# Performance work log

Measured on AMD Instinct MI355X. Metric: run time of the kernel, lower is better.

The kernel has to match this reference:

```python
import jax, jax.numpy as jnp
import numpy as np

B, S, HID = 1, 2048, 1024
H, HKV, D = 16, 4, 64
THETA = 10000.0


def _rope_tables(seq_len, head_dim):
    # Matches RotaryEmbedding: emb = cat(freqs, freqs); kernel reads cos/sin at even
    # positions d for each rotated pair (d, d+1), i.e. columns 0::2 of the table.
    inv_freq = 1.0 / (THETA ** (jnp.arange(0, head_dim, 2, dtype=jnp.float32) / head_dim))
    freqs = jnp.arange(seq_len, dtype=jnp.float32)[:, None] * inv_freq[None, :]  # [S, D/2]
    emb = jnp.concatenate([freqs, freqs], axis=-1)  # [S, D]
    return jnp.cos(emb)[:, 0::2], jnp.sin(emb)[:, 0::2]  # each [S, D/2]


def _apply_rope(x, cos, sin):
    # x: [B, H, S, D]; rotate interleaved pairs (2i, 2i+1) as in the kernel.
    xe, xo = x[..., 0::2], x[..., 1::2]
    re = xe * cos - xo * sin
    ro = xe * sin + xo * cos
    return jnp.stack([re, ro], axis=-1).reshape(x.shape)


def setup_inputs() -> dict:
    key = jax.random.key(0)
    k0, k1, k2, k3, k4 = jax.random.split(key, 5)
    return {
        "hidden_states": jax.random.normal(k0, (B, S, HID), dtype=jnp.float32),
        "Wq": jax.random.normal(k1, (HID, H * D), dtype=jnp.float32) * 0.02,
        "Wk": jax.random.normal(k2, (HID, HKV * D), dtype=jnp.float32) * 0.02,
        "Wv": jax.random.normal(k3, (HID, HKV * D), dtype=jnp.float32) * 0.02,
        "Wo": jax.random.normal(k4, (H * D, HID), dtype=jnp.float32) * 0.02,
    }


def reference(hidden_states, Wq, Wk, Wv, Wo):
    b, s, _ = hidden_states.shape
    q = (hidden_states @ Wq).reshape(b, s, H, D).transpose(0, 2, 1, 3)    # [B,H,S,D]
    k = (hidden_states @ Wk).reshape(b, s, HKV, D).transpose(0, 2, 1, 3)  # [B,Hkv,S,D]
    v = (hidden_states @ Wv).reshape(b, s, HKV, D).transpose(0, 2, 1, 3)

    cos, sin = _rope_tables(s, D)
    q = _apply_rope(q, cos, sin)
    k = _apply_rope(k, cos, sin)

    G = H // HKV  # GQA group size: query head h -> kv head h // G
    qg = q.reshape(b, HKV, G, s, D)
    scale = jnp.float32(D) ** -0.5
    scores = jnp.einsum("bkgqd,bkpd->bkgqp", qg, k) * scale  # [B,Hkv,G,S,S]
    causal = jnp.tril(jnp.ones((s, s), dtype=bool))
    scores = jnp.where(causal, scores, jnp.float32(-1e30))
    probs = jax.nn.softmax(scores, axis=-1)
    out = jnp.einsum("bkgqp,bkpd->bkgqd", probs, v).reshape(b, H, s, D)
    out = out.transpose(0, 2, 1, 3).reshape(b, s, H * D)
    return out @ Wo
```

## Files before the change

kernel.cpp:

```cpp
#include <hip/hip_runtime.h>
#include <hip/hip_bf16.h>
#include <math.h>

#define SEQ   2048
#define HID   1024
#define NH    16
#define NKV   4
#define DH    64
#define GQ    (NH / NKV)
#define NQKV  1536
#define KT    64
#define QB    32
#define CH    512
#define NCH   (SEQ / CH)
#define PSTR  72
#define LNSC  0.2878231366f
#define GS    528
#define BUFS  (8 * GS)
#define QSCALE 0.18033688011112042f

typedef __attribute__((ext_vector_type(8))) short bf16x8;
typedef __attribute__((ext_vector_type(4))) float f32x4;
typedef unsigned short u16;
typedef unsigned int u32;

__device__ __forceinline__ u16 f2bf(float f) {
    union { float f; unsigned u; } x; x.f = f;
    unsigned r = x.u + 0x7fffu + ((x.u >> 16) & 1u);
    return (u16)(r >> 16);
}
__device__ __forceinline__ u32 cvtpk(float lo, float hi) {
    u32 r;
    asm("v_cvt_pk_bf16_f32 %0, %1, %2" : "=v"(r) : "v"(lo), "v"(hi));
    return r;
}
__device__ __forceinline__ void load_lds16(const u16* g, u16* l) {
    __builtin_amdgcn_global_load_lds(
        (const __attribute__((address_space(1))) unsigned int*)g,
        (__attribute__((address_space(3))) unsigned int*)l, 16, 0, 0);
}

__global__ __launch_bounds__(256) void setup(const float* __restrict__ X,
                                             const float* __restrict__ Wq,
                                             const float* __restrict__ Wk,
                                             const float* __restrict__ Wv,
                                             const float* __restrict__ Wo,
                                             u16* __restrict__ Xb,
                                             u16* __restrict__ Wt,
                                             u16* __restrict__ WoT) {
    const int z = blockIdx.z;
    if (z == 4) {
        const int idx = ((int)blockIdx.y * 64 + (int)blockIdx.x) * 256 + threadIdx.x;
        const float4 v = ((const float4*)X)[idx];
        ushort4 o;
        o.x = f2bf(v.x); o.y = f2bf(v.y); o.z = f2bf(v.z); o.w = f2bf(v.w);
        ((ushort4*)Xb)[idx] = o;
        return;
    }
    const float* in; u16* out; int N;
    if (z == 0)      { in = Wq; out = Wt;                             N = HID; }
    else if (z == 1) { in = Wk; out = Wt + (size_t)HID * HID;         N = 256; }
    else if (z == 2) { in = Wv; out = Wt + (size_t)(HID + 256) * HID; N = 256; }
    else             { in = Wo; out = WoT;                            N = HID; }

    const int n0 = blockIdx.x * 32;
    if (n0 >= N) return;
    const int k0 = blockIdx.y * 32;

    __shared__ float t[32][33];
    const int tx = threadIdx.x & 31;
    const int ty = threadIdx.x >> 5;
    #pragma unroll
    for (int i = 0; i < 4; ++i)
        t[ty + i * 8][tx] = in[(size_t)(k0 + ty + i * 8) * N + n0 + tx];
    __syncthreads();
    #pragma unroll
    for (int i = 0; i < 4; ++i)
        out[(size_t)(n0 + ty + i * 8) * HID + k0 + tx] = f2bf(t[tx][ty + i * 8]);
}

__global__ __launch_bounds__(256, 3) void gemm_qkv(const u16* __restrict__ A,
                                                   const u16* __restrict__ Bt,
                                                   u16* __restrict__ Qb,
                                                   u16* __restrict__ Kb,
                                                   u16* __restrict__ VTg) {
    __shared__ u16 Bs[4 * BUFS];

    const int tid  = threadIdx.x;
    const int lane = tid & 63;
    const int w    = tid >> 6;
    const int c    = lane & 15;
    const int quad = lane >> 4;
    const int m0   = blockIdx.y * 64;
    const int n0   = blockIdx.x * 64;

    const int rr8 = lane >> 3;
    const int cc8 = lane & 7;
    const u16* gB0 = Bt + (size_t)(n0 + w * 16 + rr8) * HID + ((cc8 ^ rr8) * 8);
    const u16* gB1 = gB0 + (size_t)8 * HID;
    const int  gofs0 = (w * 2) * GS, gofs1 = (w * 2 + 1) * GS;

    const u16* gA = A + (size_t)(m0 + w * 16 + c) * HID + quad * 8;
    const int bbase = (c >> 3) * GS + (c & 7) * 64;
    int bsw[2];
    #pragma unroll
    for (int ks = 0; ks < 2; ++ks)
        bsw[ks] = bbase + (((ks * 4 + quad) ^ (c & 7)) * 8);

    f32x4 acc[4];
    #pragma unroll
    for (int nt = 0; nt < 4; ++nt) acc[nt] = (f32x4){0.f, 0.f, 0.f, 0.f};

    bf16x8 afc[2], afB[2], afn[2];
    afc[0] = *(const bf16x8*)gA;
    afc[1] = *(const bf16x8*)(gA + 32);
    load_lds16(gB0,      &Bs[0 * BUFS + gofs0]);
    load_lds16(gB1,      &Bs[0 * BUFS + gofs1]);
    load_lds16(gB0 + 64, &Bs[1 * BUFS + gofs0]);
    load_lds16(gB1 + 64, &Bs[1 * BUFS + gofs1]);

    const int NI = HID / 128;
    for (int i = 0; i < NI; ++i) {
        const int t0 = 2 * i;
        __syncthreads();
        if (i + 1 < NI) {
            load_lds16(gB0 + (t0 + 2) * 64, &Bs[((t0 + 2) & 3) * BUFS + gofs0]);
            load_lds16(gB1 + (t0 + 2) * 64, &Bs[((t0 + 2) & 3) * BUFS + gofs1]);
            load_lds16(gB0 + (t0 + 3) * 64, &Bs[((t0 + 3) & 3) * BUFS + gofs0]);
            load_lds16(gB1 + (t0 + 3) * 64, &Bs[((t0 + 3) & 3) * BUFS + gofs1]);
        }
        afB[0] = *(const bf16x8*)(gA + (t0 + 1) * 64);
        afB[1] = *(const bf16x8*)(gA + (t0 + 1) * 64 + 32);
        if (i + 1 < NI) {
            afn[0] = *(const bf16x8*)(gA + (t0 + 2) * 64);
            afn[1] = *(const bf16x8*)(gA + (t0 + 2) * 64 + 32);
        }
        {
            const int b = (t0 & 3) * BUFS;
            bf16x8 bfr[4][2];
            #pragma unroll
            for (int nt = 0; nt < 4; ++nt)
                #pragma unroll
                for (int ks = 0; ks < 2; ++ks)
                    bfr[nt][ks] = *(const bf16x8*)&Bs[b + nt * (2 * GS) + bsw[ks]];
            #pragma unroll
            for (int ks = 0; ks < 2; ++ks)
                #pragma unroll
                for (int nt = 0; nt < 4; ++nt)
                    acc[nt] = __builtin_amdgcn_mfma_f32_16x16x32_bf16(afc[ks], bfr[nt][ks], acc[nt], 0, 0, 0);
        }
        {
            const int b = ((t0 + 1) & 3) * BUFS;
            bf16x8 bfr[4][2];
            #pragma unroll
            for (int nt = 0; nt < 4; ++nt)
                #pragma unroll
                for (int ks = 0; ks < 2; ++ks)
                    bfr[nt][ks] = *(const bf16x8*)&Bs[b + nt * (2 * GS) + bsw[ks]];
            #pragma unroll
            for (int ks = 0; ks < 2; ++ks)
                #pragma unroll
                for (int nt = 0; nt < 4; ++nt)
                    acc[nt] = __builtin_amdgcn_mfma_f32_16x16x32_bf16(afB[ks], bfr[nt][ks], acc[nt], 0, 0, 0);
        }
        afc[0] = afn[0];
        afc[1] = afn[1];
    }

    const int s0 = m0 + w * 16 + quad * 4;
    if (n0 < 1280) {
        const bool isQ = (n0 < 1024);
        #pragma unroll
        for (int nt = 0; nt < 4; ++nt) {
            const int d = nt * 16 + c;
            const float inv_freq = __expf(-(float)(d & 30) * LNSC);
            const float sgn = (d & 1) ? 1.f : -1.f;
            #pragma unroll
            for (int rg = 0; rg < 4; ++rg) {
                const float self = acc[nt][rg];
                const float partner = __shfl_xor(self, 1);
                float sn, cs;
                __sincosf((float)(s0 + rg) * inv_freq, &sn, &cs);
                float o = fmaf(partner, sgn * sn, self * cs);
                if (isQ) {
                    Qb[(size_t)(s0 + rg) * HID + n0 + d] = f2bf(o * QSCALE);
                } else {
                    const int kh = (n0 - 1024) >> 6;
                    Kb[((size_t)kh * SEQ + s0 + rg) * DH + d] = f2bf(o);
                }
            }
        }
    } else {
        const int kh = (n0 - 1280) >> 6;
        #pragma unroll
        for (int nt = 0; nt < 4; ++nt) {
            const int d = nt * 16 + c;
            ushort4 o;
            o.x = f2bf(acc[nt][0]); o.y = f2bf(acc[nt][1]);
            o.z = f2bf(acc[nt][2]); o.w = f2bf(acc[nt][3]);
            *(ushort4*)&VTg[((size_t)kh * DH + d) * SEQ + s0] = o;
        }
    }
}

__global__ __launch_bounds__(256, 3) void gemm64(const u16* __restrict__ A,
                                                 const u16* __restrict__ Bt,
                                                 float* __restrict__ C,
                                                 int K, int ldc) {
    __shared__ u16 Bs[4 * BUFS];

    const int tid  = threadIdx.x;
    const int lane = tid & 63;
    const int w    = tid >> 6;
    const int c    = lane & 15;
    const int quad = lane >> 4;
    const int m0   = blockIdx.y * 64;
    const int n0   = blockIdx.x * 64;

    const int rr8 = lane >> 3;
    const int cc8 = lane & 7;
    const u16* gB0 = Bt + (size_t)(n0 + w * 16 + rr8) * K + ((cc8 ^ rr8) * 8);
    const u16* gB1 = gB0 + (size_t)8 * K;
    const int  gofs0 = (w * 2) * GS, gofs1 = (w * 2 + 1) * GS;

    const u16* gA = A + (size_t)(m0 + w * 16 + c) * K + quad * 8;
    const int bbase = (c >> 3) * GS + (c & 7) * 64;
    int bsw[2];
    #pragma unroll
    for (int ks = 0; ks < 2; ++ks)
        bsw[ks] = bbase + (((ks * 4 + quad) ^ (c & 7)) * 8);

    f32x4 acc[4];
    #pragma unroll
    for (int nt = 0; nt < 4; ++nt) acc[nt] = (f32x4){0.f, 0.f, 0.f, 0.f};

    bf16x8 afc[2], afB[2], afn[2];
    afc[0] = *(const bf16x8*)gA;
    afc[1] = *(const bf16x8*)(gA + 32);
    load_lds16(gB0,      &Bs[0 * BUFS + gofs0]);
    load_lds16(gB1,      &Bs[0 * BUFS + gofs1]);
    load_lds16(gB0 + 64, &Bs[1 * BUFS + gofs0]);
    load_lds16(gB1 + 64, &Bs[1 * BUFS + gofs1]);

    const int NI = K / 128;
    for (int i = 0; i < NI; ++i) {
        const int t0 = 2 * i;
        __syncthreads();
        if (i + 1 < NI) {
            load_lds16(gB0 + (t0 + 2) * 64, &Bs[((t0 + 2) & 3) * BUFS + gofs0]);
            load_lds16(gB1 + (t0 + 2) * 64, &Bs[((t0 + 2) & 3) * BUFS + gofs1]);
            load_lds16(gB0 + (t0 + 3) * 64, &Bs[((t0 + 3) & 3) * BUFS + gofs0]);
            load_lds16(gB1 + (t0 + 3) * 64, &Bs[((t0 + 3) & 3) * BUFS + gofs1]);
        }
        afB[0] = *(const bf16x8*)(gA + (t0 + 1) * 64);
        afB[1] = *(const bf16x8*)(gA + (t0 + 1) * 64 + 32);
        if (i + 1 < NI) {
            afn[0] = *(const bf16x8*)(gA + (t0 + 2) * 64);
            afn[1] = *(const bf16x8*)(gA + (t0 + 2) * 64 + 32);
        }
        {
            const int b = (t0 & 3) * BUFS;
            bf16x8 bfr[4][2];
            #pragma unroll
            for (int nt = 0; nt < 4; ++nt)
                #pragma unroll
                for (int ks = 0; ks < 2; ++ks)
                    bfr[nt][ks] = *(const bf16x8*)&Bs[b + nt * (2 * GS) + bsw[ks]];
            #pragma unroll
            for (int ks = 0; ks < 2; ++ks)
                #pragma unroll
                for (int nt = 0; nt < 4; ++nt)
                    acc[nt] = __builtin_amdgcn_mfma_f32_16x16x32_bf16(afc[ks], bfr[nt][ks], acc[nt], 0, 0, 0);
        }
        {
            const int b = ((t0 + 1) & 3) * BUFS;
            bf16x8 bfr[4][2];
            #pragma unroll
            for (int nt = 0; nt < 4; ++nt)
                #pragma unroll
                for (int ks = 0; ks < 2; ++ks)
                    bfr[nt][ks] = *(const bf16x8*)&Bs[b + nt * (2 * GS) + bsw[ks]];
            #pragma unroll
            for (int ks = 0; ks < 2; ++ks)
                #pragma unroll
                for (int nt = 0; nt < 4; ++nt)
                    acc[nt] = __builtin_amdgcn_mfma_f32_16x16x32_bf16(afB[ks], bfr[nt][ks], acc[nt], 0, 0, 0);
        }
        afc[0] = afn[0];
        afc[1] = afn[1];
    }

    #pragma unroll
    for (int nt = 0; nt < 4; ++nt)
        #pragma unroll
        for (int rg = 0; rg < 4; ++rg)
            C[(size_t)(m0 + w * 16 + quad * 4 + rg) * ldc + n0 + nt * 16 + c] = acc[nt][rg];
}

__global__ __launch_bounds__(256) void attn_kernel(const u16* __restrict__ Qb,
                                                   const u16* __restrict__ Kb,
                                                   const u16* __restrict__ VTg,
                                                   float* __restrict__ Opart,
                                                   float* __restrict__ lpart,
                                                   u16* __restrict__ At) {
    __shared__ u16 Ks[2][64 * 64];
    __shared__ u16 Vs[2][64 * 64];
    __shared__ u16 Pst[4][QB * PSTR];

    const int tid  = threadIdx.x;
    const int lane = tid & 63;
    const int w    = tid >> 6;
    const int c    = lane & 15;
    const int quad = lane >> 4;
    const int kh   = blockIdx.y;
    const int z    = blockIdx.z;
    const int qt   = (SEQ / QB - 1) - (int)blockIdx.x;
    const int q0   = qt * QB;
    const int h    = kh * GQ + w;

    const int kstart = z * CH;
    const int klim   = q0 + QB;
    if (kstart >= klim) return;
    const int kend   = (klim < kstart + CH) ? klim : (kstart + CH);
    const int ntiles = (kend - kstart + KT - 1) / KT;

    bf16x8 qf[2][2];
    #pragma unroll
    for (int g = 0; g < 2; ++g)
        #pragma unroll
        for (int ks = 0; ks < 2; ++ks)
            qf[g][ks] = *(const bf16x8*)&Qb[(size_t)(q0 + g * 16 + c) * HID + h * DH + ks * 32 + quad * 8];

    f32x4 accO[4][2];
    #pragma unroll
    for (int nt = 0; nt < 4; ++nt)
        #pragma unroll
        for (int g = 0; g < 2; ++g)
            accO[nt][g] = (f32x4){0.f, 0.f, 0.f, 0.f};
    float l[2] = {0.f, 0.f};

    const int rr = lane >> 3;
    const int sw = ((lane & 7) ^ rr) * 8;

    #pragma unroll
    for (int gi = 0; gi < 2; ++gi) {
        const int row = w * 16 + gi * 8;
        load_lds16(Kb + ((size_t)kh * SEQ + kstart + row + rr) * DH + sw,
                   &Ks[0][row * 64]);
        load_lds16(VTg + ((size_t)kh * DH + row + rr) * SEQ + kstart + sw,
                   &Vs[0][row * 64]);
    }

    for (int t = 0; t < ntiles; ++t) {
        const int kt0 = kstart + t * KT;
        __syncthreads();
        if (t + 1 < ntiles) {
            const int nk = kt0 + KT;
            const int nb = (t + 1) & 1;
            #pragma unroll
            for (int gi = 0; gi < 2; ++gi) {
                const int row = w * 16 + gi * 8;
                load_lds16(Kb + ((size_t)kh * SEQ + nk + row + rr) * DH + sw,
                           &Ks[nb][row * 64]);
                load_lds16(VTg + ((size_t)kh * DH + row + rr) * SEQ + nk + sw,
                           &Vs[nb][row * 64]);
            }
        }
        const int b = t & 1;

        f32x4 accS[4][2];
        #pragma unroll
        for (int nS = 0; nS < 4; ++nS)
            #pragma unroll
            for (int g = 0; g < 2; ++g)
                accS[nS][g] = (f32x4){0.f, 0.f, 0.f, 0.f};
        #pragma unroll
        for (int nS = 0; nS < 4; ++nS)
            #pragma unroll
            for (int ks = 0; ks < 2; ++ks) {
                const bf16x8 kf = *(const bf16x8*)
                    &Ks[b][(nS * 16 + c) * 64 + (((ks * 4 + quad) ^ (c & 7)) * 8)];
                #pragma unroll
                for (int g = 0; g < 2; ++g)
                    accS[nS][g] = __builtin_amdgcn_mfma_f32_16x16x32_bf16(kf, qf[g][ks], accS[nS][g], 0, 0, 0);
            }

        #pragma unroll
        for (int g = 0; g < 2; ++g) {
            const int q = q0 + g * 16 + c;
            const bool full = (kt0 + KT - 1 <= q0 + g * 16);
            #pragma unroll
            for (int nS = 0; nS < 4; ++nS) {
                const int key = kt0 + nS * 16 + quad * 4;
                float p0, p1, p2, p3;
                if (full) {
                    p0 = __builtin_amdgcn_exp2f(accS[nS][g][0]);
                    p1 = __builtin_amdgcn_exp2f(accS[nS][g][1]);
                    p2 = __builtin_amdgcn_exp2f(accS[nS][g][2]);
                    p3 = __builtin_amdgcn_exp2f(accS[nS][g][3]);
                } else {
                    p0 = (key + 0 <= q) ? __builtin_amdgcn_exp2f(accS[nS][g][0]) : 0.f;
                    p1 = (key + 1 <= q) ? __builtin_amdgcn_exp2f(accS[nS][g][1]) : 0.f;
                    p2 = (key + 2 <= q) ? __builtin_amdgcn_exp2f(accS[nS][g][2]) : 0.f;
                    p3 = (key + 3 <= q) ? __builtin_amdgcn_exp2f(accS[nS][g][3]) : 0.f;
                }
                l[g] += (p0 + p1) + (p2 + p3);
                u32* dst = (u32*)&Pst[w][(g * 16 + c) * PSTR + nS * 16 + quad * 4];
                dst[0] = cvtpk(p0, p1);
                dst[1] = cvtpk(p2, p3);
            }
        }
        __threadfence_block();

        #pragma unroll
        for (int ks2 = 0; ks2 < 2; ++ks2) {
            bf16x8 pf[2];
            #pragma unroll
            for (int g = 0; g < 2; ++g)
                pf[g] = *(const bf16x8*)&Pst[w][(g * 16 + c) * PSTR + ks2 * 32 + quad * 8];
            #pragma unroll
            for (int nt = 0; nt < 4; ++nt) {
                const bf16x8 vf = *(const bf16x8*)
                    &Vs[b][(nt * 16 + c) * 64 + (((ks2 * 4 + quad) ^ (c & 7)) * 8)];
                #pragma unroll
                for (int g = 0; g < 2; ++g)
                    accO[nt][g] = __builtin_amdgcn_mfma_f32_16x16x32_bf16(vf, pf[g], accO[nt][g], 0, 0, 0);
            }
        }
    }

    const int nchunks = (q0 + QB + CH - 1) / CH;

    if (nchunks == 1) {
        #pragma unroll
        for (int g = 0; g < 2; ++g) {
            float lg = l[g];
            lg += __shfl_xor(lg, 16);
            lg += __shfl_xor(lg, 32);
            const float inv = 1.0f / lg;
            u16* Ap = At + (size_t)(q0 + g * 16 + c) * HID + h * DH;
            #pragma unroll
            for (int nt = 0; nt < 4; ++nt) {
                ushort4 o;
                o.x = f2bf(accO[nt][g][0] * inv);
                o.y = f2bf(accO[nt][g][1] * inv);
                o.z = f2bf(accO[nt][g][2] * inv);
                o.w = f2bf(accO[nt][g][3] * inv);
                *(ushort4*)&Ap[nt * 16 + quad * 4] = o;
            }
        }
        return;
    }

    #pragma unroll
    for (int g = 0; g < 2; ++g) {
        float lg = l[g];
        lg += __shfl_xor(lg, 16);
        lg += __shfl_xor(lg, 32);
        if (quad == 0)
            lpart[((size_t)z * SEQ + q0 + g * 16 + c) * NH + h] = lg;

        float* Op = Opart + ((size_t)z * SEQ + q0 + g * 16 + c) * HID + h * DH;
        #pragma unroll
        for (int nt = 0; nt < 4; ++nt)
            *(f32x4*)&Op[nt * 16 + quad * 4] = accO[nt][g];
    }
}

__global__ __launch_bounds__(256) void attn_reduce(const float* __restrict__ Opart,
                                                   const float* __restrict__ lpart,
                                                   u16* __restrict__ At) {
    const int idx = blockIdx.x * 256 + threadIdx.x + (CH * HID / 4);
    const int q  = idx >> 8;
    const int h  = (idx & 255) >> 4;
    const int klim = (q & ~(QB - 1)) + QB;
    float4 o = ((const float4*)Opart)[idx];
    float  l = lpart[q * NH + h];
    #pragma unroll
    for (int z = 1; z < NCH; ++z) {
        if (z * CH < klim) {
            const float4 o1 = ((const float4*)Opart)[idx + z * (SEQ * HID / 4)];
            o.x += o1.x; o.y += o1.y; o.z += o1.z; o.w += o1.w;
            l += lpart[(z * SEQ + q) * NH + h];
        }
    }
    const float inv = 1.0f / l;
    ushort4 r;
    r.x = f2bf(o.x * inv); r.y = f2bf(o.y * inv);
    r.z = f2bf(o.z * inv); r.w = f2bf(o.w * inv);
    ((ushort4*)At)[idx] = r;
}

extern "C" void kernel_launch(void* const* d_in, const int* in_sizes, int n_in,
                              void* d_out, int out_size, void* d_ws, size_t ws_size,
                              hipStream_t stream) {
    const float* X  = (const float*)d_in[0];
    const float* Wq = (const float*)d_in[1];
    const float* Wk = (const float*)d_in[2];
    const float* Wv = (const float*)d_in[3];
    const float* Wo = (const float*)d_in[4];
    float* out = (float*)d_out;

    u16* Wt     = (u16*)d_ws;
    u16* WoT    = Wt + (size_t)NQKV * HID;
    u16* Xb     = WoT + (size_t)HID * HID;
    u16* At     = Xb + (size_t)SEQ * HID;
    u16* Qb     = At + (size_t)SEQ * HID;
    u16* Kb     = Qb + (size_t)SEQ * HID;
    u16* VTg    = Kb + (size_t)NKV * SEQ * DH;
    float* Opart = (float*)(VTg + (size_t)NKV * DH * SEQ);
    float* lpart = Opart + (size_t)NCH * SEQ * HID;

    dim3 blk(256);

    setup<<<dim3(64, 32, 5), blk, 0, stream>>>(X, Wq, Wk, Wv, Wo, Xb, Wt, WoT);

    gemm_qkv<<<dim3(NQKV / 64, SEQ / 64), blk, 0, stream>>>(Xb, Wt, Qb, Kb, VTg);

    attn_kernel<<<dim3(SEQ / QB, NKV, NCH), blk, 0, stream>>>(Qb, Kb, VTg, Opart, lpart, At);

    attn_reduce<<<((SEQ - CH) * HID / 4) / 256, blk, 0, stream>>>(Opart, lpart, At);

    gemm64<<<dim3(HID / 64, SEQ / 64), blk, 0, stream>>>(At, WoT, out, HID, HID);
}
```

Measured before the change: 132.0 us.

## Fuse split-K attention reduction into attention kernel via last-block ticket counter

Removes the separate attn_reduce launch. Each attention block fences its partial output, takes a ticket from a per-(query tile, kv head) atomic counter, and the last-arriving chunk sums the partial O and l across chunks, normalizes, and writes bf16 At. The counters are zeroed in the setup kernel. This saves a kernel launch and some re-reads, at the cost of atomics, fences, and a serialized tail reduction inside the last block of each tile.

```diff
diff --git a/kernel.cpp b/kernel.cpp
--- a/kernel.cpp
+++ b/kernel.cpp
@@ -47,9 +47,12 @@
                                              const float* __restrict__ Wo,
                                              u16* __restrict__ Xb,
                                              u16* __restrict__ Wt,
-                                             u16* __restrict__ WoT) {
+                                             u16* __restrict__ WoT,
+                                             u32* __restrict__ cnt) {
     const int z = blockIdx.z;
     if (z == 4) {
+        if (blockIdx.x == 0 && blockIdx.y == 0)
+            cnt[threadIdx.x] = 0;
         const int idx = ((int)blockIdx.y * 64 + (int)blockIdx.x) * 256 + threadIdx.x;
         const float4 v = ((const float4*)X)[idx];
         ushort4 o;
@@ -302,10 +305,12 @@
                                                    const u16* __restrict__ VTg,
                                                    float* __restrict__ Opart,
                                                    float* __restrict__ lpart,
-                                                   u16* __restrict__ At) {
+                                                   u16* __restrict__ At,
+                                                   u32* __restrict__ cnt) {
     __shared__ u16 Ks[2][64 * 64];
     __shared__ u16 Vs[2][64 * 64];
     __shared__ u16 Pst[4][QB * PSTR];
+    __shared__ u32 ticket;
 
     const int tid  = threadIdx.x;
     const int lane = tid & 63;
@@ -465,30 +470,34 @@
         for (int nt = 0; nt < 4; ++nt)
             *(f32x4*)&Op[nt * 16 + quad * 4] = accO[nt][g];
     }
-}
-
-__global__ __launch_bounds__(256) void attn_reduce(const float* __restrict__ Opart,
-                                                   const float* __restrict__ lpart,
-                                                   u16* __restrict__ At) {
-    const int idx = blockIdx.x * 256 + threadIdx.x + (CH * HID / 4);
-    const int q  = idx >> 8;
-    const int h  = (idx & 255) >> 4;
-    const int klim = (q & ~(QB - 1)) + QB;
-    float4 o = ((const float4*)Opart)[idx];
-    float  l = lpart[q * NH + h];
-    #pragma unroll
-    for (int z = 1; z < NCH; ++z) {
-        if (z * CH < klim) {
-            const float4 o1 = ((const float4*)Opart)[idx + z * (SEQ * HID / 4)];
+
+    __threadfence();
+    __syncthreads();
+    if (tid == 0) ticket = atomicAdd(&cnt[qt * NKV + kh], 1u);
+    __syncthreads();
+    if (ticket != (u32)(nchunks - 1)) return;
+    __threadfence();
+
+    const int mrow = q0 + (tid >> 3);
+    const int colbase = kh * (GQ * DH);
+    #pragma unroll
+    for (int it = 0; it < 8; ++it) {
+        const int f4 = (tid & 7) + it * 8;
+        const int mh = kh * GQ + (f4 >> 4);
+        float4 o = {0.f, 0.f, 0.f, 0.f};
+        float lsum = 0.f;
+        for (int zz = 0; zz < nchunks; ++zz) {
+            const float4 o1 = *(const float4*)
+                &Opart[((size_t)zz * SEQ + mrow) * HID + colbase + f4 * 4];
             o.x += o1.x; o.y += o1.y; o.z += o1.z; o.w += o1.w;
-            l += lpart[(z * SEQ + q) * NH + h];
-        }
-    }
-    const float inv = 1.0f / l;
-    ushort4 r;
-    r.x = f2bf(o.x * inv); r.y = f2bf(o.y * inv);
-    r.z = f2bf(o.z * inv); r.w = f2bf(o.w * inv);
-    ((ushort4*)At)[idx] = r;
+            lsum += lpart[((size_t)zz * SEQ + mrow) * NH + mh];
+        }
+        const float inv = 1.0f / lsum;
+        ushort4 r;
+        r.x = f2bf(o.x * inv); r.y = f2bf(o.y * inv);
+        r.z = f2bf(o.z * inv); r.w = f2bf(o.w * inv);
+        *(ushort4*)&At[(size_t)mrow * HID + colbase + f4 * 4] = r;
+    }
 }
 
 extern "C" void kernel_launch(void* const* d_in, const int* in_sizes, int n_in,
@@ -510,16 +519,15 @@
     u16* VTg    = Kb + (size_t)NKV * SEQ * DH;
     float* Opart = (float*)(VTg + (size_t)NKV * DH * SEQ);
     float* lpart = Opart + (size_t)NCH * SEQ * HID;
+    u32*   cnt   = (u32*)(lpart + (size_t)NCH * SEQ * NH);
 
     dim3 blk(256);
 
-    setup<<<dim3(64, 32, 5), blk, 0, stream>>>(X, Wq, Wk, Wv, Wo, Xb, Wt, WoT);
+    setup<<<dim3(64, 32, 5), blk, 0, stream>>>(X, Wq, Wk, Wv, Wo, Xb, Wt, WoT, cnt);
 
     gemm_qkv<<<dim3(NQKV / 64, SEQ / 64), blk, 0, stream>>>(Xb, Wt, Qb, Kb, VTg);
 
-    attn_kernel<<<dim3(SEQ / QB, NKV, NCH), blk, 0, stream>>>(Qb, Kb, VTg, Opart, lpart, At);
-
-    attn_reduce<<<((SEQ - CH) * HID / 4) / 256, blk, 0, stream>>>(Opart, lpart, At);
+    attn_kernel<<<dim3(SEQ / QB, NKV, NCH), blk, 0, stream>>>(Qb, Kb, VTg, Opart, lpart, At, cnt);
 
     gemm64<<<dim3(HID / 64, SEQ / 64), blk, 0, stream>>>(At, WoT, out, HID, HID);
 }
```

Result: slower. 231.7 us (+75.6%).
